# Performance work log

Hardware: AMD Instinct MI355X
Metric: run time of the kernel (lower is better)

Reference implementation:

```python
import jax, jax.numpy as jnp
import numpy as np

B, T, F, H = 128, 200, 171, 1024
GT_NUM, COND_NUM = 5, 5


def _condition_mask(seq_len, gt_num, cond_num):
    period = np.concatenate([np.ones(gt_num), np.zeros(cond_num)])
    reps = int(np.ceil(seq_len / period.size))
    return jnp.asarray(np.tile(period, reps)[:seq_len] > 0.5)


def setup_inputs() -> dict:
    key = jax.random.key(0)
    ks = jax.random.split(key, 16)
    s = 0.03  # small init for numerical stability of the recurrence
    return {
        "real_seq": jax.random.normal(ks[0], (B, T, F), jnp.float32),
        "W_ih1": jax.random.normal(ks[1], (4 * H, F), jnp.float32) * s,
        "b_ih1": jax.random.normal(ks[2], (4 * H,), jnp.float32) * s,
        "W_hh1": jax.random.normal(ks[3], (4 * H, H), jnp.float32) * s,
        "b_hh1": jax.random.normal(ks[4], (4 * H,), jnp.float32) * s,
        "W_ih2": jax.random.normal(ks[5], (4 * H, H), jnp.float32) * s,
        "b_ih2": jax.random.normal(ks[6], (4 * H,), jnp.float32) * s,
        "W_hh2": jax.random.normal(ks[7], (4 * H, H), jnp.float32) * s,
        "b_hh2": jax.random.normal(ks[8], (4 * H,), jnp.float32) * s,
        "W_ih3": jax.random.normal(ks[9], (4 * H, H), jnp.float32) * s,
        "b_ih3": jax.random.normal(ks[10], (4 * H,), jnp.float32) * s,
        "W_hh3": jax.random.normal(ks[11], (4 * H, H), jnp.float32) * s,
        "b_hh3": jax.random.normal(ks[12], (4 * H,), jnp.float32) * s,
        "W_dec": jax.random.normal(ks[13], (F, H), jnp.float32) * s,
        "b_dec": jax.random.normal(ks[14], (F,), jnp.float32) * s,
    }


def _lstm_cell(x, h, c, W_ih, b_ih, W_hh, b_hh):
    # PyTorch LSTMCell: gates ordered i, f, g, o
    gates = x @ W_ih.T + b_ih + h @ W_hh.T + b_hh
    i, f, g, o = jnp.split(gates, 4, axis=-1)
    c_new = jax.nn.sigmoid(f) * c + jax.nn.sigmoid(i) * jnp.tanh(g)
    h_new = jax.nn.sigmoid(o) * jnp.tanh(c_new)
    return h_new, c_new


def reference(real_seq, W_ih1, b_ih1, W_hh1, b_hh1, W_ih2, b_ih2, W_hh2, b_hh2,
              W_ih3, b_ih3, W_hh3, b_hh3, W_dec, b_dec):
    batch, seq_len, _ = real_seq.shape
    hs = W_hh1.shape[1]
    cond = _condition_mask(seq_len, GT_NUM, COND_NUM)  # [T] bool
    z = jnp.zeros((batch, hs), real_seq.dtype)
    out0 = jnp.zeros((batch, W_dec.shape[0]), real_seq.dtype)

    def step(carry, xs):
        h0, h1, h2, c0, c1, c2, prev_out = carry
        x_t, use_gt = xs
        in_frame = jnp.where(use_gt, x_t, prev_out)
        h0, c0 = _lstm_cell(in_frame, h0, c0, W_ih1, b_ih1, W_hh1, b_hh1)
        h1, c1 = _lstm_cell(h0, h1, c1, W_ih2, b_ih2, W_hh2, b_hh2)
        h2, c2 = _lstm_cell(h1, h2, c2, W_ih3, b_ih3, W_hh3, b_hh3)
        out = h2 @ W_dec.T + b_dec
        return (h0, h1, h2, c0, c1, c2, out), out

    xs = (jnp.swapaxes(real_seq, 0, 1), cond)  # [T,B,F], [T]
    _, outs = jax.lax.scan(step, (z, z, z, z, z, z, out0), xs)
    # outs: [T, B, F] -> match torch.cat over dim=1: [B, T*F]
    return jnp.swapaxes(outs, 0, 1).reshape(batch, -1)
```

## Files before the change

kernel.cpp:

```cpp
#include <hip/hip_runtime.h>

typedef unsigned short u16;
typedef __attribute__((ext_vector_type(8))) short bf16x8;
typedef __attribute__((ext_vector_type(4))) float f32x4;

#define MFMA(a,b,c) __builtin_amdgcn_mfma_f32_16x16x32_bf16(a,b,c,0,0,0)

#define B_   128
#define T_   200
#define F_   171
#define FX_  256
#define H_   1024
#define G_   4096
#define TF_  (T_*F_)
#define BH_  (B_*H_)
#define NB_  256
#define NT_  512

__device__ __forceinline__ u16 f2bf(float v){
  union { float f; unsigned u; } c; c.f = v;
  unsigned r = (c.u + 0x7fffu + ((c.u >> 16) & 1u)) >> 16;
  return (u16)r;
}
__device__ __forceinline__ float bf2f(u16 h){
  union { unsigned u; float f; } c; c.u = ((unsigned)h) << 16; return c.f;
}
__device__ __forceinline__ bf16x8 ld8(const u16* p){
  return *reinterpret_cast<const bf16x8*>(p);
}
__device__ __forceinline__ void st2a(u16* p, u16 v){
  __hip_atomic_store(p, v, __ATOMIC_RELAXED, __HIP_MEMORY_SCOPE_AGENT);
}
__device__ __forceinline__ void st4a(float* p, float v){
  __hip_atomic_store(p, v, __ATOMIC_RELAXED, __HIP_MEMORY_SCOPE_AGENT);
}
__device__ __forceinline__ float sigm(float v){ return 1.f / (1.f + __expf(-v)); }


__device__ __forceinline__ void gbar(unsigned* bar, unsigned ep, int tid,
                                     bool leader, unsigned xcd,
                                     unsigned n_my, unsigned x_act){
  __syncthreads();
  if (tid == 0){
    unsigned* leaf = bar + xcd*16;
    unsigned* root = bar + 256;
    unsigned* flag = bar + 272 + xcd*16;
    const unsigned r = __hip_atomic_fetch_add(leaf, 1u, __ATOMIC_RELAXED, __HIP_MEMORY_SCOPE_AGENT);
    if (r == ep * n_my - 1u)
      __hip_atomic_fetch_add(root, 1u, __ATOMIC_RELAXED, __HIP_MEMORY_SCOPE_AGENT);
    if (leader){
      while (__hip_atomic_load(root, __ATOMIC_RELAXED, __HIP_MEMORY_SCOPE_AGENT) < ep * x_act)
        __builtin_amdgcn_s_sleep(1);
      __builtin_amdgcn_fence(__ATOMIC_ACQUIRE, "agent");
      __hip_atomic_store(flag, ep, __ATOMIC_RELEASE, __HIP_MEMORY_SCOPE_AGENT);
    } else {
      while (__hip_atomic_load(flag, __ATOMIC_RELAXED, __HIP_MEMORY_SCOPE_AGENT) < ep)
        __builtin_amdgcn_s_sleep(1);
    }
  }
  asm volatile("" ::: "memory");
  __syncthreads();
}

template<int KC, int TPR>
__device__ __forceinline__ void gemm_red_f(
    const bf16x8* wreg, const u16* __restrict__ hb,
    int kcg0, int lane, int w, int r16, int ke, float (*red)[128][20])
{
  f32x4 acc[8];
#pragma unroll
  for (int bt = 0; bt < 8; ++bt) acc[bt] = (f32x4){0,0,0,0};
#pragma unroll
  for (int kc = 0; kc < KC; ++kc){
#pragma unroll
    for (int bt = 0; bt < 8; ++bt){
      const int off = (bt*TPR + kcg0 + kc)*512 + lane*8;
      acc[bt] = MFMA(ld8(hb + off), wreg[kc], acc[bt]);
    }
  }
#pragma unroll
  for (int bt = 0; bt < 8; ++bt)
#pragma unroll
    for (int e = 0; e < 4; ++e)
      red[w][bt*16 + ke*4 + e][r16] = acc[bt][e];
}

__device__ __forceinline__ void cell_update(
    const float* bias4, float& c, bool addgp,
    u16* __restrict__ ohh,
    int bid, int bl, int u2, float (*red)[128][20], float (*gp)[16])
{
  float g[4];
#pragma unroll
  for (int q = 0; q < 4; ++q){
    float s = bias4[q];
#pragma unroll
    for (int ww = 0; ww < 8; ++ww) s += red[ww][bl][q*4 + u2];
    if (addgp) s += gp[bl][q*4 + u2];
    g[q] = s;
  }
  const float cn = sigm(g[1])*c + sigm(g[0])*tanhf(g[2]);
  const float hn = sigm(g[3])*tanhf(cn);
  c = cn;
  const int col = bid*4 + u2;
  const int idx = ((bl >> 4)*32 + (col >> 5))*512 + ((col >> 3) & 3)*128
                + (bl & 15)*8 + (col & 7);
  st2a(ohh + idx, f2bf(hn));
}

__global__ __attribute__((amdgpu_flat_work_group_size(NT_, NT_)))
           __attribute__((amdgpu_waves_per_eu(2, 2)))
void k_main(
    const float* __restrict__ x, float* __restrict__ out,
    const u16* __restrict__ W1X, const u16* __restrict__ W1H,
    const u16* __restrict__ W2,  const u16* __restrict__ W3,
    const u16* __restrict__ WD,
    const float* __restrict__ bperm, const float* __restrict__ bdec,
    u16* __restrict__ h_hi, u16* __restrict__ if_hi,
    unsigned* __restrict__ bar)
{
  const int tid = threadIdx.x, bid = blockIdx.x;
  const int w = tid >> 6, lane = tid & 63, r16 = lane & 15, ke = lane >> 4;
  const int bl = tid >> 2, u2 = tid & 3;
  __shared__ float red[8][128][20];
  __shared__ float gp[128][16];
  __shared__ unsigned s_info[3];

  unsigned xcc; asm volatile("s_getreg_b32 %0, hwreg(HW_REG_XCC_ID)" : "=s"(xcc));
  xcc &= 15;
  if (tid == 0){
    unsigned* chk   = bar + 528;
    unsigned* iroot = bar + 560;
    const unsigned rank = __hip_atomic_fetch_add(&chk[xcc], 1u, __ATOMIC_RELAXED, __HIP_MEMORY_SCOPE_AGENT);
    __builtin_amdgcn_fence(__ATOMIC_RELEASE, "agent");
    __hip_atomic_fetch_add(iroot, 1u, __ATOMIC_RELAXED, __HIP_MEMORY_SCOPE_AGENT);
    while (__hip_atomic_load(iroot, __ATOMIC_RELAXED, __HIP_MEMORY_SCOPE_AGENT) < (unsigned)NB_)
      __builtin_amdgcn_s_sleep(1);
    __builtin_amdgcn_fence(__ATOMIC_ACQUIRE, "agent");
    unsigned xact = 0;
    for (int i = 0; i < 16; ++i)
      xact += (__hip_atomic_load(&chk[i], __ATOMIC_RELAXED, __HIP_MEMORY_SCOPE_AGENT) != 0u);
    s_info[0] = rank;
    s_info[1] = __hip_atomic_load(&chk[xcc], __ATOMIC_RELAXED, __HIP_MEMORY_SCOPE_AGENT);
    s_info[2] = xact;
  }
  __syncthreads();
  const bool leader = (s_info[0] == 0u);
  const unsigned n_my = s_info[1], x_act = s_info[2];

  const size_t wrow = (size_t)(bid*16 + r16);
  bf16x8 w2r[8], w3r[8], w1h[4], w1x, wdr[4];
#pragma unroll
  for (int kc = 0; kc < 8; ++kc) w2r[kc] = ld8(W2 + wrow*2048 + w*256 + kc*32 + ke*8);
#pragma unroll
  for (int kc = 0; kc < 8; ++kc) w3r[kc] = ld8(W3 + wrow*2048 + w*256 + kc*32 + ke*8);
#pragma unroll
  for (int kc = 0; kc < 4; ++kc) w1h[kc] = ld8(W1H + wrow*1024 + w*128 + kc*32 + ke*8);
  w1x = ld8(W1X + wrow*FX_ + w*32 + ke*8);

  const int dct = bid >> 3, db = bid & 7;
  const float bd = (bid < 88) ? bdec[dct*16 + (tid & 15)] : 0.f;
  if (bid < 88){
#pragma unroll
    for (int kc = 0; kc < 4; ++kc)
      wdr[kc] = ld8(WD + (size_t)(dct*16 + r16)*1024 + w*128 + kc*32 + ke*8);
  } else {
#pragma unroll
    for (int kc = 0; kc < 4; ++kc) wdr[kc] = (bf16x8){0,0,0,0,0,0,0,0};
  }

  float bias[3][4], cs[3] = {0.f, 0.f, 0.f};
#pragma unroll
  for (int l = 0; l < 3; ++l)
#pragma unroll
    for (int q = 0; q < 4; ++q) bias[l][q] = bperm[l*G_ + bid*16 + q*4 + u2];

  for (int i = tid; i < 128*16; i += NT_) gp[i >> 4][i & 15] = 0.f;
  __syncthreads();

  unsigned ep = 0;
  for (int t = 0; t < T_; ++t){
    const int cur = t & 1, prv = cur ^ 1;
    u16* h0c = h_hi + (0*2+cur)*BH_;
    u16* h1c = h_hi + (1*2+cur)*BH_;
    u16* h2c = h_hi + (2*2+cur)*BH_;
    const u16* h1p = h_hi + (1*2+prv)*BH_;
    const u16* h2p = h_hi + (2*2+prv)*BH_;

    gemm_red_f<1, 8>(&w1x, if_hi, w, lane, w, r16, ke, red);
    __syncthreads();
    cell_update(bias[0], cs[0], true, h0c, bid, bl, u2, red, gp);
    ++ep; gbar(bar, ep, tid, leader, xcc, n_my, x_act);

    if (w < 4) gemm_red_f<8, 32>(w2r, h0c, w*8,     lane, w, r16, ke, red);
    else       gemm_red_f<8, 32>(w2r, h1p, (w-4)*8, lane, w, r16, ke, red);
    __syncthreads();
    cell_update(bias[1], cs[1], false, h1c, bid, bl, u2, red, gp);
    ++ep; gbar(bar, ep, tid, leader, xcc, n_my, x_act);

    if (w < 4) gemm_red_f<8, 32>(w3r, h1c, w*8,     lane, w, r16, ke, red);
    else       gemm_red_f<8, 32>(w3r, h2p, (w-4)*8, lane, w, r16, ke, red);
    __syncthreads();
    cell_update(bias[2], cs[2], false, h2c, bid, bl, u2, red, gp);
    ++ep; gbar(bar, ep, tid, leader, xcc, n_my, x_act);

    gemm_red_f<4, 32>(w1h, h0c, w*4, lane, w, r16, ke, red);
    __syncthreads();
#pragma unroll
    for (int q = 0; q < 4; ++q){
      float s = 0.f;
#pragma unroll
      for (int ww = 0; ww < 8; ++ww) s += red[ww][bl][q*4 + u2];
      gp[bl][q*4 + u2] = s;
    }
    if (bid < 88){
      __syncthreads();
      f32x4 dacc = {0,0,0,0};
#pragma unroll
      for (int kc = 0; kc < 4; ++kc){
        const int off = (db*32 + w*4 + kc)*512 + lane*8;
        dacc = MFMA(ld8(h2c + off), wdr[kc], dacc);
      }
#pragma unroll
      for (int e = 0; e < 4; ++e) red[w][ke*4 + e][r16] = dacc[e];
      __syncthreads();
      if (tid < 256){
        const int bl2 = tid >> 4, fl = tid & 15;
        float v = bd;
#pragma unroll
        for (int ww = 0; ww < 8; ++ww) v += red[ww][bl2][fl];
        const int f = dct*16 + fl, b = db*16 + bl2;
        if (f < F_){
          st4a(out + (size_t)b*TF_ + (size_t)t*F_ + f, v);
          if (t + 1 < T_){
            const bool gt = (((t+1) % 10) < 5);
            const float in = gt ? x[(size_t)b*TF_ + (size_t)(t+1)*F_ + f] : v;
            const int idx2 = (db*8 + (f >> 5))*512 + ((f >> 3) & 3)*128 + bl2*8 + (f & 7);
            st2a(if_hi + idx2, f2bf(in));
          }
        }
      }
    }
    ++ep; gbar(bar, ep, tid, leader, xcc, n_my, x_act);
  }
}

__global__ void k_prep(const float* __restrict__ x,
                       const float* bi1, const float* bh1,
                       const float* bi2, const float* bh2,
                       const float* bi3, const float* bh3,
                       const float* bd_in,
                       float* __restrict__ bperm, float* __restrict__ bdec,
                       u16* __restrict__ if_hi)
{
  const int i = blockIdx.x * blockDim.x + threadIdx.x;
  if (i < 3*G_){
    const int l = i >> 12, r = i & 4095;
    const int blk = r >> 4, g = (r >> 2) & 3, u2 = r & 3;
    const int j = (g << 10) | (blk << 2) | u2;
    const float* bi = (l == 0) ? bi1 : (l == 1) ? bi2 : bi3;
    const float* bh = (l == 0) ? bh1 : (l == 1) ? bh2 : bh3;
    bperm[i] = bi[j] + bh[j];
  }
  const int i2 = i - 3*G_;
  if (i2 >= 0 && i2 < 192) bdec[i2] = (i2 < F_) ? bd_in[i2] : 0.f;
  const int i3 = i2 - 192;
  if (i3 >= 0 && i3 < B_*FX_){
    const int b = i3 >> 8, f = i3 & 255;
    const float v = (f < F_) ? x[(size_t)b*TF_ + f] : 0.f;
    const int idx = ((b >> 4)*8 + (f >> 5))*512 + ((f >> 3) & 3)*128 + (b & 15)*8 + (f & 7);
    if_hi[idx] = f2bf(v);
  }
}

__global__ void k_wcvt(const float* __restrict__ Wih1, const float* __restrict__ Whh1,
                       const float* __restrict__ Wih2, const float* __restrict__ Whh2,
                       const float* __restrict__ Wih3, const float* __restrict__ Whh3,
                       const float* __restrict__ Wd_in,
                       u16* __restrict__ W1X, u16* __restrict__ W1H,
                       u16* __restrict__ W2,  u16* __restrict__ W3,
                       u16* __restrict__ WD)
{
  const int region = blockIdx.y;
  const size_t stride = (size_t)gridDim.x * blockDim.x;
  const size_t i0 = (size_t)blockIdx.x * blockDim.x + threadIdx.x;
  if (region == 0){
    for (size_t i = i0; i < (size_t)G_*FX_; i += stride){
      const int r = (int)(i >> 8), k = (int)(i & 255);
      const int blk = r >> 4, g = (r >> 2) & 3, u2 = r & 3;
      const int j = (g << 10) | (blk << 2) | u2;
      W1X[i] = f2bf((k < F_) ? Wih1[(size_t)j*F_ + k] : 0.f);
    }
  } else if (region == 1){
    for (size_t i = i0; i < (size_t)G_*H_; i += stride){
      const int r = (int)(i >> 10), k = (int)(i & 1023);
      const int blk = r >> 4, g = (r >> 2) & 3, u2 = r & 3;
      const int j = (g << 10) | (blk << 2) | u2;
      W1H[i] = f2bf(Whh1[(size_t)j*H_ + k]);
    }
  } else if (region == 2){
    for (size_t i = i0; i < (size_t)G_*2048; i += stride){
      const int r = (int)(i >> 11), k = (int)(i & 2047);
      const int blk = r >> 4, g = (r >> 2) & 3, u2 = r & 3;
      const int j = (g << 10) | (blk << 2) | u2;
      W2[i] = f2bf((k < H_) ? Wih2[(size_t)j*H_ + k] : Whh2[(size_t)j*H_ + (k - H_)]);
    }
  } else if (region == 3){
    for (size_t i = i0; i < (size_t)G_*2048; i += stride){
      const int r = (int)(i >> 11), k = (int)(i & 2047);
      const int blk = r >> 4, g = (r >> 2) & 3, u2 = r & 3;
      const int j = (g << 10) | (blk << 2) | u2;
      W3[i] = f2bf((k < H_) ? Wih3[(size_t)j*H_ + k] : Whh3[(size_t)j*H_ + (k - H_)]);
    }
  } else {
    for (size_t i = i0; i < (size_t)176*H_; i += stride){
      const int r = (int)(i >> 10), k = (int)(i & 1023);
      WD[i] = f2bf((r < F_) ? Wd_in[(size_t)r*H_ + k] : 0.f);
    }
  }
}

extern "C" void kernel_launch(void* const* d_in, const int* in_sizes, int n_in,
                              void* d_out, int out_size, void* d_ws, size_t ws_size,
                              hipStream_t stream)
{
  const float* x    = (const float*)d_in[0];
  const float* Wih1 = (const float*)d_in[1];
  const float* bih1 = (const float*)d_in[2];
  const float* Whh1 = (const float*)d_in[3];
  const float* bhh1 = (const float*)d_in[4];
  const float* Wih2 = (const float*)d_in[5];
  const float* bih2 = (const float*)d_in[6];
  const float* Whh2 = (const float*)d_in[7];
  const float* bhh2 = (const float*)d_in[8];
  const float* Wih3 = (const float*)d_in[9];
  const float* bih3 = (const float*)d_in[10];
  const float* Whh3 = (const float*)d_in[11];
  const float* bhh3 = (const float*)d_in[12];
  const float* Wdec = (const float*)d_in[13];
  const float* bdec_in = (const float*)d_in[14];
  float* out = (float*)d_out;

  char* ws = (char*)d_ws;
  size_t off = 0;
  auto alloc = [&](size_t bytes) -> void* {
    void* p = ws + off;
    off = (off + bytes + 255) & ~(size_t)255;
    return p;
  };
  unsigned* bar = (unsigned*)alloc(4096);
  u16* h_hi  = (u16*)alloc((size_t)3*2*BH_*2);
  u16* if_hi = (u16*)alloc((size_t)B_*FX_*2);
  const size_t zero_bytes = off;
  u16* W1X = (u16*)alloc((size_t)G_*FX_*2);
  u16* W1H = (u16*)alloc((size_t)G_*H_*2);
  u16* W2  = (u16*)alloc((size_t)G_*2048*2);
  u16* W3  = (u16*)alloc((size_t)G_*2048*2);
  u16* WD  = (u16*)alloc((size_t)176*H_*2);
  float* bperm = (float*)alloc((size_t)3*G_*4);
  float* bdec  = (float*)alloc((size_t)192*4);

  hipMemsetAsync(d_ws, 0, zero_bytes, stream);
  k_prep<<<180, 256, 0, stream>>>(x, bih1, bhh1, bih2, bhh2, bih3, bhh3, bdec_in,
                                  bperm, bdec, if_hi);
  k_wcvt<<<dim3(2048, 5), 256, 0, stream>>>(Wih1, Whh1, Wih2, Whh2, Wih3, Whh3, Wdec,
                                            W1X, W1H, W2, W3, WD);
  k_main<<<NB_, NT_, 0, stream>>>(x, out, W1X, W1H, W2, W3, WD, bperm, bdec,
                                  h_hi, if_hi, bar);
}
```

Before: 10.49 ms.

## Replicate decoder per XCD and replace final grid barrier with local XCD barrier

Each XCD now redundantly computes the full decoder output (11 ranked blocks per XCD covering all batches) into its own private copy of the next-step input buffer. That lets the fourth per-timestep barrier be a cheap XCD-local barrier instead of a device-wide one. The global barrier also drops its two-level root counter: the leader now polls all 16 leaf counters directly. The cost is redundant decoder MFMA work and writes to out from every XCD. The scheme also assumes each XCD holds at least 11 blocks and that all 16 XCD slots exist (it waits for ep*256).

```diff
diff --git a/kernel.cpp b/kernel.cpp
--- a/kernel.cpp
+++ b/kernel.cpp
@@ -38,25 +38,40 @@
 
 
 __device__ __forceinline__ void gbar(unsigned* bar, unsigned ep, int tid,
-                                     bool leader, unsigned xcd,
-                                     unsigned n_my, unsigned x_act){
+                                     bool leader, unsigned xcd){
   __syncthreads();
   if (tid == 0){
     unsigned* leaf = bar + xcd*16;
-    unsigned* root = bar + 256;
     unsigned* flag = bar + 272 + xcd*16;
-    const unsigned r = __hip_atomic_fetch_add(leaf, 1u, __ATOMIC_RELAXED, __HIP_MEMORY_SCOPE_AGENT);
-    if (r == ep * n_my - 1u)
-      __hip_atomic_fetch_add(root, 1u, __ATOMIC_RELAXED, __HIP_MEMORY_SCOPE_AGENT);
+    __hip_atomic_fetch_add(leaf, 1u, __ATOMIC_RELAXED, __HIP_MEMORY_SCOPE_AGENT);
     if (leader){
-      while (__hip_atomic_load(root, __ATOMIC_RELAXED, __HIP_MEMORY_SCOPE_AGENT) < ep * x_act)
+      for (;;){
+        unsigned s = 0;
+#pragma unroll
+        for (int i = 0; i < 16; ++i)
+          s += __hip_atomic_load(bar + i*16, __ATOMIC_RELAXED, __HIP_MEMORY_SCOPE_AGENT);
+        if (s >= ep * (unsigned)NB_) break;
         __builtin_amdgcn_s_sleep(1);
+      }
       __builtin_amdgcn_fence(__ATOMIC_ACQUIRE, "agent");
       __hip_atomic_store(flag, ep, __ATOMIC_RELEASE, __HIP_MEMORY_SCOPE_AGENT);
     } else {
       while (__hip_atomic_load(flag, __ATOMIC_RELAXED, __HIP_MEMORY_SCOPE_AGENT) < ep)
         __builtin_amdgcn_s_sleep(1);
     }
+  }
+  asm volatile("" ::: "memory");
+  __syncthreads();
+}
+
+__device__ __forceinline__ void lbar(unsigned* bar, unsigned ep2, int tid,
+                                     unsigned xcd, unsigned n_my){
+  __syncthreads();
+  if (tid == 0){
+    unsigned* c = bar + 768 + xcd*16;
+    __hip_atomic_fetch_add(c, 1u, __ATOMIC_RELAXED, __HIP_MEMORY_SCOPE_AGENT);
+    while (__hip_atomic_load(c, __ATOMIC_RELAXED, __HIP_MEMORY_SCOPE_AGENT) < ep2 * n_my)
+      __builtin_amdgcn_s_sleep(1);
   }
   asm volatile("" ::: "memory");
   __syncthreads();
@@ -116,7 +131,7 @@
     const u16* __restrict__ W2,  const u16* __restrict__ W3,
     const u16* __restrict__ WD,
     const float* __restrict__ bperm, const float* __restrict__ bdec,
-    u16* __restrict__ h_hi, u16* __restrict__ if_hi,
+    u16* __restrict__ h_hi, u16* __restrict__ if_base,
     unsigned* __restrict__ bar)
 {
   const int tid = threadIdx.x, bid = blockIdx.x;
@@ -137,16 +152,15 @@
     while (__hip_atomic_load(iroot, __ATOMIC_RELAXED, __HIP_MEMORY_SCOPE_AGENT) < (unsigned)NB_)
       __builtin_amdgcn_s_sleep(1);
     __builtin_amdgcn_fence(__ATOMIC_ACQUIRE, "agent");
-    unsigned xact = 0;
-    for (int i = 0; i < 16; ++i)
-      xact += (__hip_atomic_load(&chk[i], __ATOMIC_RELAXED, __HIP_MEMORY_SCOPE_AGENT) != 0u);
     s_info[0] = rank;
     s_info[1] = __hip_atomic_load(&chk[xcc], __ATOMIC_RELAXED, __HIP_MEMORY_SCOPE_AGENT);
-    s_info[2] = xact;
-  }
-  __syncthreads();
-  const bool leader = (s_info[0] == 0u);
-  const unsigned n_my = s_info[1], x_act = s_info[2];
+    s_info[2] = 0;
+  }
+  __syncthreads();
+  const unsigned rank = s_info[0];
+  const bool leader = (rank == 0u);
+  const unsigned n_my = s_info[1];
+  u16* if_own = if_base + (size_t)xcc * (B_ * FX_);
 
   const size_t wrow = (size_t)(bid*16 + r16);
   bf16x8 w2r[8], w3r[8], w1h[4], w1x, wdr[4];
@@ -157,13 +171,10 @@
 #pragma unroll
   for (int kc = 0; kc < 4; ++kc) w1h[kc] = ld8(W1H + wrow*1024 + w*128 + kc*32 + ke*8);
   w1x = ld8(W1X + wrow*FX_ + w*32 + ke*8);
-
-  const int dct = bid >> 3, db = bid & 7;
-  const float bd = (bid < 88) ? bdec[dct*16 + (tid & 15)] : 0.f;
-  if (bid < 88){
+  if (rank < 11u){
 #pragma unroll
     for (int kc = 0; kc < 4; ++kc)
-      wdr[kc] = ld8(WD + (size_t)(dct*16 + r16)*1024 + w*128 + kc*32 + ke*8);
+      wdr[kc] = ld8(WD + (size_t)(rank*16 + r16)*1024 + w*128 + kc*32 + ke*8);
   } else {
 #pragma unroll
     for (int kc = 0; kc < 4; ++kc) wdr[kc] = (bf16x8){0,0,0,0,0,0,0,0};
@@ -178,7 +189,7 @@
   for (int i = tid; i < 128*16; i += NT_) gp[i >> 4][i & 15] = 0.f;
   __syncthreads();
 
-  unsigned ep = 0;
+  unsigned ep = 0, ep2 = 0;
   for (int t = 0; t < T_; ++t){
     const int cur = t & 1, prv = cur ^ 1;
     u16* h0c = h_hi + (0*2+cur)*BH_;
@@ -187,22 +198,22 @@
     const u16* h1p = h_hi + (1*2+prv)*BH_;
     const u16* h2p = h_hi + (2*2+prv)*BH_;
 
-    gemm_red_f<1, 8>(&w1x, if_hi, w, lane, w, r16, ke, red);
+    gemm_red_f<1, 8>(&w1x, if_own, w, lane, w, r16, ke, red);
     __syncthreads();
     cell_update(bias[0], cs[0], true, h0c, bid, bl, u2, red, gp);
-    ++ep; gbar(bar, ep, tid, leader, xcc, n_my, x_act);
+    ++ep; gbar(bar, ep, tid, leader, xcc);
 
     if (w < 4) gemm_red_f<8, 32>(w2r, h0c, w*8,     lane, w, r16, ke, red);
     else       gemm_red_f<8, 32>(w2r, h1p, (w-4)*8, lane, w, r16, ke, red);
     __syncthreads();
     cell_update(bias[1], cs[1], false, h1c, bid, bl, u2, red, gp);
-    ++ep; gbar(bar, ep, tid, leader, xcc, n_my, x_act);
+    ++ep; gbar(bar, ep, tid, leader, xcc);
 
     if (w < 4) gemm_red_f<8, 32>(w3r, h1c, w*8,     lane, w, r16, ke, red);
     else       gemm_red_f<8, 32>(w3r, h2p, (w-4)*8, lane, w, r16, ke, red);
     __syncthreads();
     cell_update(bias[2], cs[2], false, h2c, bid, bl, u2, red, gp);
-    ++ep; gbar(bar, ep, tid, leader, xcc, n_my, x_act);
+    ++ep; gbar(bar, ep, tid, leader, xcc);
 
     gemm_red_f<4, 32>(w1h, h0c, w*4, lane, w, r16, ke, red);
     __syncthreads();
@@ -213,35 +224,46 @@
       for (int ww = 0; ww < 8; ++ww) s += red[ww][bl][q*4 + u2];
       gp[bl][q*4 + u2] = s;
     }
-    if (bid < 88){
+    if (rank < 11u){
       __syncthreads();
-      f32x4 dacc = {0,0,0,0};
+      f32x4 dacc[8];
+#pragma unroll
+      for (int bt = 0; bt < 8; ++bt) dacc[bt] = (f32x4){0,0,0,0};
 #pragma unroll
       for (int kc = 0; kc < 4; ++kc){
-        const int off = (db*32 + w*4 + kc)*512 + lane*8;
-        dacc = MFMA(ld8(h2c + off), wdr[kc], dacc);
+#pragma unroll
+        for (int bt = 0; bt < 8; ++bt){
+          const int off = (bt*32 + w*4 + kc)*512 + lane*8;
+          dacc[bt] = MFMA(ld8(h2c + off), wdr[kc], dacc[bt]);
+        }
       }
 #pragma unroll
-      for (int e = 0; e < 4; ++e) red[w][ke*4 + e][r16] = dacc[e];
+      for (int bt = 0; bt < 8; ++bt)
+#pragma unroll
+        for (int e = 0; e < 4; ++e)
+          red[w][bt*16 + ke*4 + e][r16] = dacc[bt][e];
       __syncthreads();
-      if (tid < 256){
-        const int bl2 = tid >> 4, fl = tid & 15;
-        float v = bd;
-#pragma unroll
-        for (int ww = 0; ww < 8; ++ww) v += red[ww][bl2][fl];
-        const int f = dct*16 + fl, b = db*16 + bl2;
+#pragma unroll
+      for (int j = 0; j < 4; ++j){
+        const int idx = tid + j*NT_;
+        const int b = idx >> 4, fl = idx & 15;
+        float v = bdec[rank*16 + fl];
+#pragma unroll
+        for (int ww = 0; ww < 8; ++ww) v += red[ww][b][fl];
+        const int f = rank*16 + fl;
         if (f < F_){
           st4a(out + (size_t)b*TF_ + (size_t)t*F_ + f, v);
           if (t + 1 < T_){
             const bool gt = (((t+1) % 10) < 5);
             const float in = gt ? x[(size_t)b*TF_ + (size_t)(t+1)*F_ + f] : v;
-            const int idx2 = (db*8 + (f >> 5))*512 + ((f >> 3) & 3)*128 + bl2*8 + (f & 7);
-            st2a(if_hi + idx2, f2bf(in));
+            const int idx2 = ((b >> 4)*8 + (f >> 5))*512 + ((f >> 3) & 3)*128
+                           + (b & 15)*8 + (f & 7);
+            if_own[idx2] = f2bf(in);
           }
         }
       }
     }
-    ++ep; gbar(bar, ep, tid, leader, xcc, n_my, x_act);
+    ++ep2; lbar(bar, ep2, tid, xcc, n_my);
   }
 }
 
@@ -251,7 +273,7 @@
                        const float* bi3, const float* bh3,
                        const float* bd_in,
                        float* __restrict__ bperm, float* __restrict__ bdec,
-                       u16* __restrict__ if_hi)
+                       u16* __restrict__ if_base)
 {
   const int i = blockIdx.x * blockDim.x + threadIdx.x;
   if (i < 3*G_){
@@ -265,11 +287,13 @@
   const int i2 = i - 3*G_;
   if (i2 >= 0 && i2 < 192) bdec[i2] = (i2 < F_) ? bd_in[i2] : 0.f;
   const int i3 = i2 - 192;
-  if (i3 >= 0 && i3 < B_*FX_){
-    const int b = i3 >> 8, f = i3 & 255;
+  if (i3 >= 0 && i3 < 16*B_*FX_){
+    const int copy = i3 >> 15, rem = i3 & 32767;
+    const int b = rem >> 8, f = rem & 255;
     const float v = (f < F_) ? x[(size_t)b*TF_ + f] : 0.f;
-    const int idx = ((b >> 4)*8 + (f >> 5))*512 + ((f >> 3) & 3)*128 + (b & 15)*8 + (f & 7);
-    if_hi[idx] = f2bf(v);
+    const int idx = copy*32768 + ((b >> 4)*8 + (f >> 5))*512 + ((f >> 3) & 3)*128
+                  + (b & 15)*8 + (f & 7);
+    if_base[idx] = f2bf(v);
   }
 }
 
@@ -349,8 +373,8 @@
     return p;
   };
   unsigned* bar = (unsigned*)alloc(4096);
-  u16* h_hi  = (u16*)alloc((size_t)3*2*BH_*2);
-  u16* if_hi = (u16*)alloc((size_t)B_*FX_*2);
+  u16* h_hi    = (u16*)alloc((size_t)3*2*BH_*2);
+  u16* if_base = (u16*)alloc((size_t)16*B_*FX_*2);
   const size_t zero_bytes = off;
   u16* W1X = (u16*)alloc((size_t)G_*FX_*2);
   u16* W1H = (u16*)alloc((size_t)G_*H_*2);
@@ -361,10 +385,10 @@
   float* bdec  = (float*)alloc((size_t)192*4);
 
   hipMemsetAsync(d_ws, 0, zero_bytes, stream);
-  k_prep<<<180, 256, 0, stream>>>(x, bih1, bhh1, bih2, bhh2, bih3, bhh3, bdec_in,
-                                  bperm, bdec, if_hi);
+  k_prep<<<2097, 256, 0, stream>>>(x, bih1, bhh1, bih2, bhh2, bih3, bhh3, bdec_in,
+                                   bperm, bdec, if_base);
   k_wcvt<<<dim3(2048, 5), 256, 0, stream>>>(Wih1, Whh1, Wih2, Whh2, Wih3, Whh3, Wdec,
                                             W1X, W1H, W2, W3, WD);
   k_main<<<NB_, NT_, 0, stream>>>(x, out, W1X, W1H, W2, W3, WD, bperm, bdec,
-                                  h_hi, if_hi, bar);
-}
+                                  h_hi, if_base, bar);
+}
```

New measurement: 13.27 ms. +26.5%, slower.
